# Kernel tuning notes

Hardware: AMD Instinct MI355X
Metric: run time of the kernel (lower is better)

## Reference

```python
import jax, jax.numpy as jnp
from jax import lax
import numpy as np

INF = 1e10


def _fps_indices(xyz, npoint, start):
    """Farthest point sampling. xyz:(B,N,3), start:(B,) int32 -> (B,npoint) indices."""
    B, N, _ = xyz.shape

    def step(carry, _):
        distance, farthest = carry  # (B,N), (B,)
        # gather current centroid: (B,1,3)
        centroid = xyz[jnp.arange(B), farthest][:, None, :]
        dist = jnp.sum((xyz - centroid) ** 2, axis=-1)  # (B,N)
        distance = jnp.minimum(distance, dist)  # torch where(dist<distance, dist, distance)
        new_farthest = jnp.argmax(distance, axis=-1)
        return (distance, new_farthest), farthest

    init_dist = jnp.full((B, N), INF, dtype=xyz.dtype)
    (_, _), centroids = lax.scan(step, (init_dist, start), None, length=npoint)
    return centroids.T  # (B, npoint)


def setup_inputs() -> dict:
    key = jax.random.key(0)
    B, N = 16, 131072
    xyz = jax.random.normal(key, (B, N, 3), dtype=jnp.float32)
    return {"xyz": xyz, "npoint": 1024}


def reference(xyz, npoint):
    B, N, _ = xyz.shape
    # torch code picks a random starting index per batch; use a fixed jax PRNG
    start = jax.random.randint(jax.random.fold_in(jax.random.key(0), 1), (B,), 0, N)
    idx = _fps_indices(xyz, npoint, start)  # (B, npoint) int
    new_xyz = xyz[jnp.arange(B)[:, None], idx]  # (B, npoint, 3)
    return new_xyz, idx
```

## Files before the change

### kernel.cpp

```cpp
#include <hip/hip_runtime.h>
#include <stdint.h>

#define NB    16
#define WPB   16
#define NTHR  512
#define NWAVE (NTHR / 64)
#define PPT   16

__device__ __forceinline__ void tf2x32(uint32_t k0, uint32_t k1,
                                       uint32_t x0, uint32_t x1,
                                       uint32_t &y0, uint32_t &y1) {
  uint32_t ks2 = k0 ^ k1 ^ 0x1BD11BDAu;
  uint32_t v0 = x0 + k0, v1 = x1 + k1;
#define TFR(r) { v0 += v1; v1 = (v1 << (r)) | (v1 >> (32 - (r))); v1 ^= v0; }
  TFR(13) TFR(15) TFR(26) TFR(6)   v0 += k1;  v1 += ks2 + 1u;
  TFR(17) TFR(29) TFR(16) TFR(24)  v0 += ks2; v1 += k0 + 2u;
  TFR(13) TFR(15) TFR(26) TFR(6)   v0 += k0;  v1 += k1 + 3u;
  TFR(17) TFR(29) TFR(16) TFR(24)  v0 += k1;  v1 += ks2 + 4u;
  TFR(13) TFR(15) TFR(26) TFR(6)   v0 += ks2; v1 += k0 + 5u;
#undef TFR
  y0 = v0; y1 = v1;
}


__attribute__((amdgpu_flat_work_group_size(512, 512)))
__attribute__((amdgpu_waves_per_eu(2, 2)))
__global__ void FPSampler_42099269435595_kernel(const float* __restrict__ xyz,
                                     const int* __restrict__ npoint_ptr,
                                     float* __restrict__ out,
                                     unsigned long long* __restrict__ slots,
                                     int N) {
#pragma clang fp contract(off)
  const int blk  = blockIdx.x;
  const int b    = blk >> 4;
  const int w    = blk & (WPB - 1);
  const int tid  = threadIdx.x;
  const int wave = tid >> 6;
  const int lane = tid & 63;
  const int npoint = npoint_ptr[0];

  const float* __restrict__ xb = xyz + (size_t)b * N * 3;
  const int p0 = w * (N / WPB) + tid;

  float px[PPT], py[PPT], pz[PPT], dist[PPT];
#pragma unroll
  for (int k = 0; k < PPT; ++k) {
    size_t p = (size_t)(p0 + k * NTHR);
    px[k] = xb[3 * p + 0];
    py[k] = xb[3 * p + 1];
    pz[k] = xb[3 * p + 2];
    dist[k] = 1e10f;
  }

  uint32_t fk0, fk1, s0, s1, r0, r1;
  tf2x32(0u, 0u, 0u, 1u, fk0, fk1);
  tf2x32(fk0, fk1, 0u, 1u, s0, s1);
  tf2x32(s0, s1, 0u, (uint32_t)b, r0, r1);
  uint32_t far = (r0 ^ r1) & 0x1FFFFu;

  float cx = xb[3 * (size_t)far + 0];
  float cy = xb[3 * (size_t)far + 1];
  float cz = xb[3 * (size_t)far + 2];

  __shared__ unsigned long long lds_key[NWAVE];
  __shared__ float lds_x[NWAVE], lds_y[NWAVE], lds_z[NWAVE];
  __shared__ unsigned int lds_bfar;
  __shared__ float lds_bcx, lds_bcy, lds_bcz;

  float* out_xyz = out;
  float* out_idx = out + (size_t)NB * npoint * 3;

  for (int i = 0; i < npoint; ++i) {
    if (w == 0 && tid == NTHR - 1) {
      size_t o = (size_t)b * npoint + i;
      out_xyz[3 * o + 0] = cx;
      out_xyz[3 * o + 1] = cy;
      out_xyz[3 * o + 2] = cz;
      out_idx[o] = (float)far;
    }
    if (i == npoint - 1) break;

    float best = -1.0f, bx = 0.f, by = 0.f, bz = 0.f;
    uint32_t bidx = 0;
#pragma unroll
    for (int k = 0; k < PPT; ++k) {
      float dx = px[k] - cx, dy = py[k] - cy, dz = pz[k] - cz;
      float d = (dx * dx + dy * dy) + dz * dz;
      float nd = fminf(dist[k], d);
      dist[k] = nd;
      if (nd > best) {
        best = nd; bidx = (uint32_t)(p0 + k * NTHR);
        bx = px[k]; by = py[k]; bz = pz[k];
      }
    }

    unsigned long long mykey =
        ((unsigned long long)__float_as_uint(best) << 19) |
        (unsigned long long)(0x7FFFFu - bidx);
    unsigned long long pk = mykey;
#pragma unroll
    for (int off = 32; off >= 1; off >>= 1) {
      unsigned long long o = __shfl_xor(pk, off);
      if (o > pk) pk = o;
    }
    unsigned long long bal = __ballot(mykey == pk);
    int wl = __ffsll(bal) - 1;
    float wx = __shfl(bx, wl), wy = __shfl(by, wl), wz = __shfl(bz, wl);
    if (lane == 0) {
      lds_key[wave] = pk;
      lds_x[wave] = wx; lds_y[wave] = wy; lds_z[wave] = wz;
    }
    __syncthreads();

    unsigned long long* base =
        slots + (size_t)((i & 1) * NB + b) * (WPB * 4);
    const uint32_t tag = (uint32_t)(i + 1);

    if (wave == 0) {
      unsigned long long k8 = (lane < NWAVE) ? lds_key[lane] : 0ull;
      unsigned long long m8 = k8;
#pragma unroll
      for (int off = 4; off >= 1; off >>= 1) {
        unsigned long long o = __shfl_xor(m8, off);
        if (o > m8) m8 = o;
      }
      unsigned long long bal8 = __ballot(lane < NWAVE && k8 == m8);
      int wv = __ffsll(bal8) - 1;

      unsigned long long wrd = 0;
      if (lane == 0) wrd = ((unsigned long long)tag << 51) | m8;
      if (lane == 1) wrd = ((unsigned long long)__float_as_uint(lds_x[wv]) << 32) | tag;
      if (lane == 2) wrd = ((unsigned long long)__float_as_uint(lds_y[wv]) << 32) | tag;
      if (lane == 3) wrd = ((unsigned long long)__float_as_uint(lds_z[wv]) << 32) | tag;
      if (lane < 4)
        __hip_atomic_store(base + w * 4 + lane, wrd, __ATOMIC_RELAXED,
                           __HIP_MEMORY_SCOPE_AGENT);

      unsigned long long v0 = __hip_atomic_load(base + lane, __ATOMIC_RELAXED,
                                                __HIP_MEMORY_SCOPE_AGENT);
      unsigned long long v1 = __hip_atomic_load(base + lane, __ATOMIC_RELAXED,
                                                __HIP_MEMORY_SCOPE_AGENT);
      for (;;) {
        uint32_t t = (lane & 3) ? (uint32_t)v0 : (uint32_t)(v0 >> 51);
        if (__all(t == tag)) break;
        v0 = v1;
        v1 = __hip_atomic_load(base + lane, __ATOMIC_RELAXED,
                               __HIP_MEMORY_SCOPE_AGENT);
      }
      unsigned long long v = v0;

      unsigned long long key = __shfl(v, (lane & 15) << 2);
      unsigned long long gk = key;
#pragma unroll
      for (int off = 8; off >= 1; off >>= 1) {
        unsigned long long o = __shfl_xor(gk, off);
        if (o > gk) gk = o;
      }
      unsigned long long gbal = __ballot(key == gk);
      int ws = (__ffsll(gbal) - 1) & 15;
      uint32_t nfar = 0x7FFFFu - (uint32_t)(gk & 0x7FFFFu);
      float ncx = __uint_as_float((uint32_t)(__shfl(v, (ws << 2) | 1) >> 32));
      float ncy = __uint_as_float((uint32_t)(__shfl(v, (ws << 2) | 2) >> 32));
      float ncz = __uint_as_float((uint32_t)(__shfl(v, (ws << 2) | 3) >> 32));
      if (lane == 0) {
        lds_bfar = nfar;
        lds_bcx = ncx; lds_bcy = ncy; lds_bcz = ncz;
      }
    }
    __syncthreads();
    far = lds_bfar;
    cx = lds_bcx; cy = lds_bcy; cz = lds_bcz;
  }
}

extern "C" void kernel_launch(void* const* d_in, const int* in_sizes, int n_in,
                              void* d_out, int out_size, void* d_ws, size_t ws_size,
                              hipStream_t stream) {
  const float* xyz = (const float*)d_in[0];
  const int* npoint = (const int*)d_in[1];
  int N = in_sizes[0] / (NB * 3);

  hipMemsetAsync(d_ws, 0,
                 (size_t)2 * NB * WPB * 4 * sizeof(unsigned long long),
                 stream);
  FPSampler_42099269435595_kernel<<<NB * WPB, NTHR, 0, stream>>>(
      xyz, npoint, (float*)d_out, (unsigned long long*)d_ws, N);
}
```

Before: 3.007 ms.

## Stage point coordinates in LDS as per-thread SoA segments with contiguous ownership

Each thread now owns 16 contiguous points instead of 16 points strided by the block size. It loads them with float4 global reads, transposes them into an SoA segment in LDS, and reads them back as float4 every iteration instead of keeping px/py/pz in registers. This frees 48 registers per thread but adds 12 LDS vector loads per iteration. The 208-byte padded stride is meant to avoid bank conflicts. Tie-breaking on the argmax stays the same, because the smallest index still wins through the key encoding and the strict > comparison within a thread.

```diff
diff --git a/kernel.cpp b/kernel.cpp
--- a/kernel.cpp
+++ b/kernel.cpp
@@ -6,6 +6,8 @@
 #define NTHR  512
 #define NWAVE (NTHR / 64)
 #define PPT   16
+#define SEG   208
+#define LDS_BYTES (NTHR * SEG)
 
 __device__ __forceinline__ void tf2x32(uint32_t k0, uint32_t k1,
                                        uint32_t x0, uint32_t x1,
@@ -31,6 +33,7 @@
                                      unsigned long long* __restrict__ slots,
                                      int N) {
 #pragma clang fp contract(off)
+  extern __shared__ char smem[];
   const int blk  = blockIdx.x;
   const int b    = blk >> 4;
   const int w    = blk & (WPB - 1);
@@ -40,17 +43,28 @@
   const int npoint = npoint_ptr[0];
 
   const float* __restrict__ xb = xyz + (size_t)b * N * 3;
-  const int p0 = w * (N / WPB) + tid;
-
-  float px[PPT], py[PPT], pz[PPT], dist[PPT];
-#pragma unroll
-  for (int k = 0; k < PPT; ++k) {
-    size_t p = (size_t)(p0 + k * NTHR);
-    px[k] = xb[3 * p + 0];
-    py[k] = xb[3 * p + 1];
-    pz[k] = xb[3 * p + 2];
-    dist[k] = 1e10f;
+  const int p0 = w * (N / WPB) + tid * PPT;
+
+  float4* seg4 = (float4*)(smem + tid * SEG);
+  {
+    const float4* g4 = (const float4*)(xb + 3 * (size_t)p0);
+    float fl[48];
+#pragma unroll
+    for (int j = 0; j < 12; ++j) {
+      float4 f = g4[j];
+      fl[4 * j + 0] = f.x; fl[4 * j + 1] = f.y;
+      fl[4 * j + 2] = f.z; fl[4 * j + 3] = f.w;
+    }
+#pragma unroll
+    for (int g = 0; g < 4; ++g) {
+      seg4[g]     = make_float4(fl[12*g+0], fl[12*g+3], fl[12*g+6], fl[12*g+9]);
+      seg4[4 + g] = make_float4(fl[12*g+1], fl[12*g+4], fl[12*g+7], fl[12*g+10]);
+      seg4[8 + g] = make_float4(fl[12*g+2], fl[12*g+5], fl[12*g+8], fl[12*g+11]);
+    }
   }
+  float dist[PPT];
+#pragma unroll
+  for (int k = 0; k < PPT; ++k) dist[k] = 1e10f;
 
   uint32_t fk0, fk1, s0, s1, r0, r1;
   tf2x32(0u, 0u, 0u, 1u, fk0, fk1);
@@ -83,14 +97,22 @@
     float best = -1.0f, bx = 0.f, by = 0.f, bz = 0.f;
     uint32_t bidx = 0;
 #pragma unroll
-    for (int k = 0; k < PPT; ++k) {
-      float dx = px[k] - cx, dy = py[k] - cy, dz = pz[k] - cz;
-      float d = (dx * dx + dy * dy) + dz * dz;
-      float nd = fminf(dist[k], d);
-      dist[k] = nd;
-      if (nd > best) {
-        best = nd; bidx = (uint32_t)(p0 + k * NTHR);
-        bx = px[k]; by = py[k]; bz = pz[k];
+    for (int g = 0; g < 4; ++g) {
+      float4 X = seg4[g], Y = seg4[4 + g], Z = seg4[8 + g];
+#pragma unroll
+      for (int m = 0; m < 4; ++m) {
+        float xk = (m == 0) ? X.x : (m == 1) ? X.y : (m == 2) ? X.z : X.w;
+        float yk = (m == 0) ? Y.x : (m == 1) ? Y.y : (m == 2) ? Y.z : Y.w;
+        float zk = (m == 0) ? Z.x : (m == 1) ? Z.y : (m == 2) ? Z.z : Z.w;
+        int k = 4 * g + m;
+        float dx = xk - cx, dy = yk - cy, dz = zk - cz;
+        float d = (dx * dx + dy * dy) + dz * dz;
+        float nd = fminf(dist[k], d);
+        dist[k] = nd;
+        if (nd > best) {
+          best = nd; bidx = (uint32_t)(p0 + k);
+          bx = xk; by = yk; bz = zk;
+        }
       }
     }
 
@@ -180,9 +202,12 @@
   const int* npoint = (const int*)d_in[1];
   int N = in_sizes[0] / (NB * 3);
 
+  hipFuncSetAttribute((const void*)FPSampler_42099269435595_kernel,
+                      hipFuncAttributeMaxDynamicSharedMemorySize, LDS_BYTES);
+
   hipMemsetAsync(d_ws, 0,
                  (size_t)2 * NB * WPB * 4 * sizeof(unsigned long long),
                  stream);
-  FPSampler_42099269435595_kernel<<<NB * WPB, NTHR, 0, stream>>>(
+  FPSampler_42099269435595_kernel<<<NB * WPB, NTHR, LDS_BYTES, stream>>>(
       xyz, npoint, (float*)d_out, (unsigned long long*)d_ws, N);
 }
```

Measured after the change: 3.216 ms. 7.0% more time.
